# Performance work log

Measured on AMD Instinct MI355X. Metric: run time of the kernel, lower is better.

The kernel has to match this reference:

```python
import jax, jax.numpy as jnp
import numpy as np

C = 256          # channels
K = 7            # kernel_size
GC = 16          # group_channels
G = C // GC      # groups = 16
RED = C // 4     # reduction channels = 64
EPS = 1e-5


def unfold_same(x, k):
    """torch nn.Unfold(k, stride=1, padding=(k-1)//2) -> (b, c, k*k, h, w),
    channel-major patch ordering matching torch (c, kh, kw)."""
    pad = (k - 1) // 2
    xp = jnp.pad(x, ((0, 0), (0, 0), (pad, pad), (pad, pad)))
    h, w = x.shape[2], x.shape[3]
    # fixed k*k=49 slices, vectorized over all data dims
    pats = jnp.stack([xp[:, :, i:i + h, j:j + w]
                      for i in range(k) for j in range(k)], axis=2)
    return pats  # (b, c, k*k, h, w)


def setup_inputs() -> dict:
    key = jax.random.key(0)
    ks = jax.random.split(key, 8)
    b, h, w = 2, 64, 64
    feature_map = jax.random.normal(ks[0], (b, C, h, w), jnp.float32)
    guide_map = jax.random.normal(ks[1], (b, C, h, w), jnp.float32)
    # convs1: 1x1 conv (no bias, followed by BN) + BN params + ReLU
    w1 = jax.random.normal(ks[2], (RED, C), jnp.float32) * (1.0 / np.sqrt(C))
    bn_gamma = jnp.ones((RED,), jnp.float32)
    bn_beta = jnp.zeros((RED,), jnp.float32)
    bn_mean = jax.random.normal(ks[3], (RED,), jnp.float32) * 0.1
    bn_var = jax.random.uniform(ks[4], (RED,), jnp.float32, 0.5, 1.5)
    # convs2: 1x1 conv with bias, out = K^2 * G channels
    w2 = jax.random.normal(ks[5], (K * K * G, RED), jnp.float32) * (1.0 / np.sqrt(RED))
    b2 = jax.random.normal(ks[6], (K * K * G,), jnp.float32) * 0.01
    return dict(feature_map=feature_map, guide_map=guide_map,
                w1=w1, bn_gamma=bn_gamma, bn_beta=bn_beta,
                bn_mean=bn_mean, bn_var=bn_var, w2=w2, b2=b2)


def reference(feature_map, guide_map, w1, bn_gamma, bn_beta, bn_mean, bn_var, w2, b2):
    b, _, h, w = feature_map.shape
    # kernel-generation branch: 1x1 conv -> BN (inference) -> ReLU -> 1x1 conv
    t = jnp.einsum('oc,bchw->bohw', w1, guide_map)
    scale = bn_gamma / jnp.sqrt(bn_var + EPS)
    shift = bn_beta - bn_mean * scale
    t = jax.nn.relu(t * scale[None, :, None, None] + shift[None, :, None, None])
    weight = jnp.einsum('or,brhw->bohw', w2, t) + b2[None, :, None, None]
    weight = weight.reshape(b, G, K * K, h, w)
    # involution: unfold, broadcast per-pixel kernels over group channels, reduce K^2
    pats = unfold_same(feature_map, K).reshape(b, G, GC, K * K, h, w)
    out = jnp.einsum('bgkhw,bgckhw->bgchw', weight, pats).reshape(b, C, h, w)
    return out + feature_map
```

## Files before the change

kernel.cpp:

```cpp
#include <hip/hip_runtime.h>

#define CC  256
#define HW  4096
#define HH  64
#define WW  64
#define RED 64
#define K2  49
#define NG  16
#define GCH 16

typedef __attribute__((ext_vector_type(8))) short bf16x8;
typedef __attribute__((ext_vector_type(4))) float f32x4;

__device__ inline unsigned short f2bf(float f) {
    union { float f; unsigned u; } v; v.f = f;
    unsigned r = v.u + 0x7FFF + ((v.u >> 16) & 1);
    return (unsigned short)(r >> 16);
}

__device__ inline float dpp_shr1(float x) {
    union { float f; int i; } v; v.f = x;
    v.i = __builtin_amdgcn_mov_dpp(v.i, 0x111, 0xf, 0xf, true);
    return v.f;
}
__device__ inline float dpp_shl1(float x) {
    union { float f; int i; } v; v.f = x;
    v.i = __builtin_amdgcn_mov_dpp(v.i, 0x101, 0xf, 0xf, true);
    return v.f;
}

#define TT_ELTS   524288
#define W2BF_ROWS 832

__global__ __launch_bounds__(128) void k1_kernel(
    const float* __restrict__ guide,
    const float* __restrict__ w1,
    const float* __restrict__ gamma,
    const float* __restrict__ beta,
    const float* __restrict__ mean,
    const float* __restrict__ var,
    const float* __restrict__ w2,
    unsigned short* __restrict__ tt,
    unsigned short* __restrict__ w2bf)
{
    const int lane = threadIdx.x & 63;
    const int unit = blockIdx.x * 2 + __builtin_amdgcn_readfirstlane(threadIdx.x >> 6);

    if (unit >= 512) {
        const int idx = (unit - 512) * 64 + lane;
        if (idx < (W2BF_ROWS * RED) / 8) {
            unsigned short r8[8];
            if (idx * 8 < K2 * NG * RED) {
                const float4 a = *reinterpret_cast<const float4*>(w2 + idx * 8);
                const float4 b = *reinterpret_cast<const float4*>(w2 + idx * 8 + 4);
                r8[0] = f2bf(a.x); r8[1] = f2bf(a.y); r8[2] = f2bf(a.z); r8[3] = f2bf(a.w);
                r8[4] = f2bf(b.x); r8[5] = f2bf(b.y); r8[6] = f2bf(b.z); r8[7] = f2bf(b.w);
            } else {
                #pragma unroll
                for (int i = 0; i < 8; ++i) r8[i] = 0;
            }
            *reinterpret_cast<uint4*>(w2bf + idx * 8) = *reinterpret_cast<const uint4*>(r8);
        }
        return;
    }

    const int bb = unit >> 8;
    const int y  = (unit >> 2) & 63;
    const int nt = unit & 3;
    const int lm = lane & 15;
    const int lg = lane >> 4;
    const int px = nt * 16 + lm;

    const float* gcol = guide + (size_t)bb * CC * HW + (size_t)y * WW + px;

    f32x4 acc[4] = {f32x4{0,0,0,0}, f32x4{0,0,0,0}, f32x4{0,0,0,0}, f32x4{0,0,0,0}};

    #pragma unroll
    for (int ks = 0; ks < 8; ++ks) {
        const int cbase = ks * 32 + lg * 8;
        union { unsigned short u[8]; bf16x8 v; } B;
        #pragma unroll
        for (int j = 0; j < 8; ++j)
            B.u[j] = f2bf(gcol[(size_t)(cbase + j) * HW]);
        #pragma unroll
        for (int mt = 0; mt < 4; ++mt) {
            const float* ar = w1 + (size_t)(mt * 16 + lm) * CC + cbase;
            const float4 a0 = *reinterpret_cast<const float4*>(ar);
            const float4 a1 = *reinterpret_cast<const float4*>(ar + 4);
            union { unsigned short u[8]; bf16x8 v; } A;
            A.u[0] = f2bf(a0.x); A.u[1] = f2bf(a0.y);
            A.u[2] = f2bf(a0.z); A.u[3] = f2bf(a0.w);
            A.u[4] = f2bf(a1.x); A.u[5] = f2bf(a1.y);
            A.u[6] = f2bf(a1.z); A.u[7] = f2bf(a1.w);
            acc[mt] = __builtin_amdgcn_mfma_f32_16x16x32_bf16(A.v, B.v, acc[mt], 0, 0, 0);
        }
    }

    const size_t ttrow = ((size_t)bb * HW + (size_t)y * WW + px) * RED;
    #pragma unroll
    for (int mt = 0; mt < 4; ++mt) {
        union { unsigned short u[4]; uint2 v; } R;
        #pragma unroll
        for (int rr = 0; rr < 4; ++rr) {
            const int o = mt * 16 + lg * 4 + rr;
            const float sc = gamma[o] * rsqrtf(var[o] + 1e-5f);
            const float sh = beta[o] - mean[o] * sc;
            float v = fmaf(acc[mt][rr], sc, sh);
            v = v > 0.f ? v : 0.f;
            R.u[rr] = f2bf(v);
        }
        *reinterpret_cast<uint2*>(tt + ttrow + mt * 16 + lg * 4) = R.v;
    }
}

__global__ __launch_bounds__(256, 3) void k2_inv_kernel(
    const float* __restrict__ feat,
    const unsigned short* __restrict__ tt,
    const unsigned short* __restrict__ w2bf,
    const float* __restrict__ b2,
    float* __restrict__ out)
{
    __shared__ float wg[2][K2][WW];

    const int bid = blockIdx.x;
    const int bb  = bid >> 9;
    const int yp  = (bid >> 4) & 31;
    const int g   = bid & 15;
    const int y0  = yp * 2;
    const int tid  = threadIdx.x;
    const int lane = tid & 63;
    const int wv   = __builtin_amdgcn_readfirstlane(tid >> 6);
    const int lm = lane & 15;
    const int lg = lane >> 4;
    const int obase = g * K2;

    {
        const int yh = wv >> 1;
        const int nh = wv & 1;
        const int y  = y0 + yh;
        f32x4 acc[2][4];
        #pragma unroll
        for (int h = 0; h < 2; ++h)
            #pragma unroll
            for (int mt = 0; mt < 4; ++mt) acc[h][mt] = f32x4{0, 0, 0, 0};

        #pragma unroll
        for (int h = 0; h < 2; ++h) {
            const int nt = nh * 2 + h;
            const size_t ttb = ((size_t)bb * HW + (size_t)y * WW + nt * 16 + lm) * RED + lg * 8;
            #pragma unroll
            for (int ks = 0; ks < 2; ++ks) {
                const bf16x8 bfr = *reinterpret_cast<const bf16x8*>(tt + ttb + ks * 32);
                #pragma unroll
                for (int mt = 0; mt < 4; ++mt) {
                    const bf16x8 afr = *reinterpret_cast<const bf16x8*>(
                        w2bf + (size_t)(obase + mt * 16 + lm) * RED + ks * 32 + lg * 8);
                    acc[h][mt] = __builtin_amdgcn_mfma_f32_16x16x32_bf16(afr, bfr, acc[h][mt], 0, 0, 0);
                }
            }
        }
        #pragma unroll
        for (int h = 0; h < 2; ++h)
            #pragma unroll
            for (int mt = 0; mt < 4; ++mt)
                #pragma unroll
                for (int rr = 0; rr < 4; ++rr) {
                    const int o2 = mt * 16 + lg * 4 + rr;
                    if (o2 < K2)
                        wg[yh][o2][nh * 32 + h * 16 + lm] = acc[h][mt][rr] + b2[obase + o2];
                }
    }
    __syncthreads();

    const int cl = tid >> 4;
    const int xq = tid & 15;
    const int x0 = xq * 4;
    const int c  = g * GCH + cl;
    const float* fb = feat + ((size_t)bb * CC + c) * HW;

    float s[2][4];
    #pragma unroll
    for (int ys = 0; ys < 2; ++ys)
        #pragma unroll
        for (int p = 0; p < 4; ++p) s[ys][p] = 0.f;

    #pragma unroll
    for (int dr = 0; dr < 8; ++dr) {
        const int r = y0 - 3 + dr;
        if (r < 0 || r >= HH) continue;
        const float* fr = fb + (size_t)r * WW;

        const float4 M = *reinterpret_cast<const float4*>(fr + x0);
        const float b1 = dpp_shr1(M.y), b2e = dpp_shr1(M.z), b3 = dpp_shr1(M.w);
        const float b8 = dpp_shl1(M.x), b9  = dpp_shl1(M.y), b10 = dpp_shl1(M.z);
        const float buf[12] = {0.f, b1, b2e, b3, M.x, M.y, M.z, M.w, b8, b9, b10, 0.f};

        #pragma unroll
        for (int ys = 0; ys < 2; ++ys) {
            const int i = dr - ys;
            if (i < 0 || i >= 7) continue;
            if (i == 3) {
                s[ys][0] += buf[4]; s[ys][1] += buf[5];
                s[ys][2] += buf[6]; s[ys][3] += buf[7];
            }
            #pragma unroll
            for (int jx = 0; jx < 7; ++jx) {
                const float4 w4 = *reinterpret_cast<const float4*>(&wg[ys][i * 7 + jx][x0]);
                s[ys][0] = fmaf(w4.x, buf[jx + 1], s[ys][0]);
                s[ys][1] = fmaf(w4.y, buf[jx + 2], s[ys][1]);
                s[ys][2] = fmaf(w4.z, buf[jx + 3], s[ys][2]);
                s[ys][3] = fmaf(w4.w, buf[jx + 4], s[ys][3]);
            }
        }
    }

    #pragma unroll
    for (int ys = 0; ys < 2; ++ys) {
        float4 o4; o4.x = s[ys][0]; o4.y = s[ys][1]; o4.z = s[ys][2]; o4.w = s[ys][3];
        *reinterpret_cast<float4*>(out + ((size_t)bb * CC + c) * HW
                                   + (size_t)(y0 + ys) * WW + x0) = o4;
    }
}

__global__ __launch_bounds__(512, 1) void crossinv_fused_kernel(
    const float* __restrict__ feat, const float* __restrict__ guide,
    const float* __restrict__ w1, const float* __restrict__ gamma,
    const float* __restrict__ beta, const float* __restrict__ mean,
    const float* __restrict__ var, const float* __restrict__ w2,
    const float* __restrict__ b2, float* __restrict__ out)
{
    __shared__ float stf[RED][WW];
    __shared__ float wgf[K2][WW];
    const int bid  = blockIdx.x;
    const int bb   = bid >> 7;
    const int y    = (bid >> 1) & 63;
    const int gsel = bid & 1;
    const int lane = threadIdx.x & 63;
    const int wv   = __builtin_amdgcn_readfirstlane(threadIdx.x >> 6);

    const float* gptr = guide + (size_t)bb * CC * HW + (size_t)y * WW + lane;
    float acc[8];
    #pragma unroll
    for (int j = 0; j < 8; ++j) acc[j] = 0.f;
    for (int c0 = 0; c0 < CC; c0 += 4) {
        const float gv0 = gptr[(c0 + 0) * HW];
        const float gv1 = gptr[(c0 + 1) * HW];
        const float gv2 = gptr[(c0 + 2) * HW];
        const float gv3 = gptr[(c0 + 3) * HW];
        #pragma unroll
        for (int j = 0; j < 8; ++j) {
            const int o = wv + 8 * j;
            const float4 wr = *reinterpret_cast<const float4*>(w1 + o * CC + c0);
            acc[j] = fmaf(wr.x, gv0, acc[j]);
            acc[j] = fmaf(wr.y, gv1, acc[j]);
            acc[j] = fmaf(wr.z, gv2, acc[j]);
            acc[j] = fmaf(wr.w, gv3, acc[j]);
        }
    }
    #pragma unroll
    for (int j = 0; j < 8; ++j) {
        const int o = wv + 8 * j;
        const float sc = gamma[o] * rsqrtf(var[o] + 1e-5f);
        const float sh = beta[o] - mean[o] * sc;
        const float v  = fmaf(acc[j], sc, sh);
        stf[o][lane] = v > 0.f ? v : 0.f;
    }
    __syncthreads();
    for (int gi = 0; gi < 8; ++gi) {
        const int gg    = gsel * 8 + gi;
        const int obase = gg * K2;
        float accw[7];
        #pragma unroll
        for (int j = 0; j < 7; ++j) {
            const int o2 = wv + 8 * j;
            accw[j] = (o2 < K2) ? b2[obase + o2] : 0.f;
        }
        for (int r0 = 0; r0 < RED; r0 += 4) {
            const float t0 = stf[r0 + 0][lane];
            const float t1 = stf[r0 + 1][lane];
            const float t2 = stf[r0 + 2][lane];
            const float t3 = stf[r0 + 3][lane];
            #pragma unroll
            for (int j = 0; j < 7; ++j) {
                const int o2 = wv + 8 * j;
                if (o2 < K2) {
                    const float4 wr = *reinterpret_cast<const float4*>(
                        w2 + (size_t)(obase + o2) * RED + r0);
                    accw[j] = fmaf(wr.x, t0, accw[j]);
                    accw[j] = fmaf(wr.y, t1, accw[j]);
                    accw[j] = fmaf(wr.z, t2, accw[j]);
                    accw[j] = fmaf(wr.w, t3, accw[j]);
                }
            }
        }
        #pragma unroll
        for (int j = 0; j < 7; ++j) {
            const int o2 = wv + 8 * j;
            if (o2 < K2) wgf[o2][lane] = accw[j];
        }
        __syncthreads();
        #pragma unroll
        for (int cc2 = 0; cc2 < 2; ++cc2) {
            const int cc = wv * 2 + cc2;
            const int cch = gg * GCH + cc;
            const float* fbp = feat + ((size_t)bb * CC + cch) * HW;
            float sum = fbp[y * WW + lane];
            #pragma unroll
            for (int i = 0; i < 7; ++i) {
                const int yy = y + i - 3;
                if (yy < 0 || yy >= HH) continue;
                const float* frow = fbp + yy * WW;
                #pragma unroll
                for (int jx = 0; jx < 7; ++jx) {
                    const int xx = lane + jx - 3;
                    const float fv = (xx >= 0 && xx < WW) ? frow[xx] : 0.f;
                    sum = fmaf(wgf[i * 7 + jx][lane], fv, sum);
                }
            }
            out[((size_t)bb * CC + cch) * HW + (size_t)y * WW + lane] = sum;
        }
        __syncthreads();
    }
}

extern "C" void kernel_launch(void* const* d_in, const int* in_sizes, int n_in,
                              void* d_out, int out_size, void* d_ws, size_t ws_size,
                              hipStream_t stream) {
    const float* feat  = (const float*)d_in[0];
    const float* guide = (const float*)d_in[1];
    const float* w1    = (const float*)d_in[2];
    const float* gamma = (const float*)d_in[3];
    const float* beta  = (const float*)d_in[4];
    const float* mean  = (const float*)d_in[5];
    const float* var   = (const float*)d_in[6];
    const float* w2    = (const float*)d_in[7];
    const float* b2    = (const float*)d_in[8];
    float* out = (float*)d_out;

    const size_t need = (size_t)TT_ELTS * 2 + (size_t)W2BF_ROWS * RED * 2;
    if (ws_size >= need) {
        unsigned short* tt   = (unsigned short*)d_ws;
        unsigned short* w2bf = tt + TT_ELTS;
        hipLaunchKernelGGL(k1_kernel, dim3(308), dim3(128), 0, stream,
                           guide, w1, gamma, beta, mean, var, w2, tt, w2bf);
        hipLaunchKernelGGL(k2_inv_kernel, dim3(1024), dim3(256), 0, stream,
                           feat, tt, w2bf, b2, out);
    } else {
        hipLaunchKernelGGL(crossinv_fused_kernel, dim3(256), dim3(512), 0, stream,
                           feat, guide, w1, gamma, beta, mean, var, w2, b2, out);
    }
}
```

Before: 24.21 us.

## Split k1 channel reduction across four waves with LDS reduction

The first kernel's 1x1 conv now gives each (batch,row,16-pixel) tile a 256-thread block. Each of the four waves handles a quarter of the 256 input channels with MFMA, and the partial sums are reduced through shared memory. After a barrier, each wave finalizes one 16-row output tile with BN+ReLU. The aim is more wave parallelism and shorter per-wave serial load chains, at the cost of an LDS round trip and a block sync. The w2 conversion blocks are remapped to 256 threads each.

Measured after the change: 25.44 us. 1.05x slower.

```diff
diff --git a/kernel.cpp b/kernel.cpp
--- a/kernel.cpp
+++ b/kernel.cpp
@@ -32,7 +32,7 @@
 #define TT_ELTS   524288
 #define W2BF_ROWS 832
 
-__global__ __launch_bounds__(128) void k1_kernel(
+__global__ __launch_bounds__(256) void k1_kernel(
     const float* __restrict__ guide,
     const float* __restrict__ w1,
     const float* __restrict__ gamma,
@@ -43,11 +43,11 @@
     unsigned short* __restrict__ tt,
     unsigned short* __restrict__ w2bf)
 {
-    const int lane = threadIdx.x & 63;
-    const int unit = blockIdx.x * 2 + __builtin_amdgcn_readfirstlane(threadIdx.x >> 6);
-
-    if (unit >= 512) {
-        const int idx = (unit - 512) * 64 + lane;
+    const int bid = blockIdx.x;
+    const int tid = threadIdx.x;
+
+    if (bid >= 512) {
+        const int idx = (bid - 512) * 256 + tid;
         if (idx < (W2BF_ROWS * RED) / 8) {
             unsigned short r8[8];
             if (idx * 8 < K2 * NG * RED) {
@@ -64,9 +64,13 @@
         return;
     }
 
-    const int bb = unit >> 8;
-    const int y  = (unit >> 2) & 63;
-    const int nt = unit & 3;
+    __shared__ float4 red[4][4][64];
+
+    const int lane = tid & 63;
+    const int wv   = __builtin_amdgcn_readfirstlane(tid >> 6);
+    const int bb = bid >> 8;
+    const int y  = (bid >> 2) & 63;
+    const int nt = bid & 3;
     const int lm = lane & 15;
     const int lg = lane >> 4;
     const int px = nt * 16 + lm;
@@ -76,7 +80,8 @@
     f32x4 acc[4] = {f32x4{0,0,0,0}, f32x4{0,0,0,0}, f32x4{0,0,0,0}, f32x4{0,0,0,0}};
 
     #pragma unroll
-    for (int ks = 0; ks < 8; ++ks) {
+    for (int kk = 0; kk < 2; ++kk) {
+        const int ks = wv * 2 + kk;
         const int cbase = ks * 32 + lg * 8;
         union { unsigned short u[8]; bf16x8 v; } B;
         #pragma unroll
@@ -96,16 +101,33 @@
         }
     }
 
-    const size_t ttrow = ((size_t)bb * HW + (size_t)y * WW + px) * RED;
     #pragma unroll
     for (int mt = 0; mt < 4; ++mt) {
+        float4 p; p.x = acc[mt][0]; p.y = acc[mt][1]; p.z = acc[mt][2]; p.w = acc[mt][3];
+        red[wv][mt][lane] = p;
+    }
+    __syncthreads();
+
+    {
+        const int mt = wv;
+        const float4 p0 = red[0][mt][lane];
+        const float4 p1 = red[1][mt][lane];
+        const float4 p2 = red[2][mt][lane];
+        const float4 p3 = red[3][mt][lane];
+        float t0 = (p0.x + p1.x) + (p2.x + p3.x);
+        float t1 = (p0.y + p1.y) + (p2.y + p3.y);
+        float t2 = (p0.z + p1.z) + (p2.z + p3.z);
+        float t3 = (p0.w + p1.w) + (p2.w + p3.w);
+
+        const size_t ttrow = ((size_t)bb * HW + (size_t)y * WW + px) * RED;
         union { unsigned short u[4]; uint2 v; } R;
+        const float tv[4] = {t0, t1, t2, t3};
         #pragma unroll
         for (int rr = 0; rr < 4; ++rr) {
             const int o = mt * 16 + lg * 4 + rr;
             const float sc = gamma[o] * rsqrtf(var[o] + 1e-5f);
             const float sh = beta[o] - mean[o] * sc;
-            float v = fmaf(acc[mt][rr], sc, sh);
+            float v = fmaf(tv[rr], sc, sh);
             v = v > 0.f ? v : 0.f;
             R.u[rr] = f2bf(v);
         }
@@ -341,7 +363,7 @@
     if (ws_size >= need) {
         unsigned short* tt   = (unsigned short*)d_ws;
         unsigned short* w2bf = tt + TT_ELTS;
-        hipLaunchKernelGGL(k1_kernel, dim3(308), dim3(128), 0, stream,
+        hipLaunchKernelGGL(k1_kernel, dim3(538), dim3(256), 0, stream,
                            guide, w1, gamma, beta, mean, var, w2, tt, w2bf);
         hipLaunchKernelGGL(k2_inv_kernel, dim3(1024), dim3(256), 0, stream,
                            feat, tt, w2bf, b2, out);
```
